# Performance work log

Measured on AMD Instinct MI355X. Metric: run time of the kernel, lower is better.

The kernel has to match this reference:

```python
import jax, jax.numpy as jnp
import numpy as np

B, C_IN, H, W = 32, 64, 64, 64
D, O, S_SP, K = 256, 512, 4, 3


def setup_inputs() -> dict:
    key = jax.random.key(0)
    k1, k2, k3, k4, k5 = jax.random.split(key, 5)
    x = jax.random.normal(k1, (B, C_IN, H, W), dtype=jnp.float32)
    dictionary = jax.random.normal(k2, (D, C_IN, K, K), dtype=jnp.float32)
    lookup_coefficients = jax.random.normal(k3, (O, S_SP), dtype=jnp.float32)
    bias = jax.random.normal(k4, (O,), dtype=jnp.float32)
    lookup_indices = jax.random.randint(k5, (O, S_SP), 0, D)
    return {
        "x": x,
        "dictionary": dictionary,
        "lookup_coefficients": lookup_coefficients,
        "bias": bias,
        "lookup_indices": lookup_indices,
    }


def reference(x, dictionary, lookup_coefficients, bias, lookup_indices):
    # Dictionary conv: S has shape [B, D, H, W] (stride 1, padding 1, 3x3 kernel)
    S = jax.lax.conv_general_dilated(
        x, dictionary,
        window_strides=(1, 1),
        padding=((1, 1), (1, 1)),
        dimension_numbers=("NCHW", "OIHW", "NCHW"),
    )
    # Build dense [O, D] combine matrix via scatter-add (duplicate indices
    # accumulate, matching the original += loop), then one GEMM.
    rows = jnp.arange(O)[:, None]  # [O, 1] broadcast against [O, sparsity]
    Wc = jnp.zeros((O, D), dtype=S.dtype).at[rows, lookup_indices].add(lookup_coefficients)
    out = jnp.einsum("bdhw,od->bohw", S, Wc)
    return out + bias[None, :, None, None]
```

## Files before the change

### kernel.cpp

```cpp
#include <hip/hip_runtime.h>
#include <stdint.h>

#define NB 32
#define NC 64
#define NH 64
#define NW 64
#define NO 512
#define HP 66

typedef __bf16 bf16x8 __attribute__((ext_vector_type(8)));
typedef short  s16x8  __attribute__((ext_vector_type(8)));
typedef float  f32x4  __attribute__((ext_vector_type(4)));

__device__ __forceinline__ uint16_t f2bf(float f) {
  uint32_t u = __builtin_bit_cast(uint32_t, f);
  u += 0x7fffu + ((u >> 16) & 1u);
  return (uint16_t)(u >> 16);
}

__device__ __forceinline__ void gld16(const uint16_t* g, uint16_t* l) {
  __builtin_amdgcn_global_load_lds(
      (const __attribute__((address_space(1))) void*)(g),
      (__attribute__((address_space(3))) void*)(l), 16, 0, 0);
}

__global__ void k_build_w(const float* __restrict__ dict,
                          const float* __restrict__ coef,
                          const int*   __restrict__ idx,
                          uint16_t*    __restrict__ Wl) {
  __shared__ float tmp[576];
  const int o = blockIdx.x;
  const int t = threadIdx.x;
  float v = 0.f;
#pragma unroll
  for (int s = 0; s < 4; ++s)
    v += coef[o * 4 + s] * dict[idx[o * 4 + s] * 576 + t];
  tmp[t] = v;
  __syncthreads();
  const int c = t & 63, p = t >> 6;
  const int sl = ((p * NO + o) * 8 + ((c >> 3) ^ (o & 7))) * 8 + (c & 7);
  Wl[sl] = f2bf(tmp[c * 9 + p]);
}

__global__ void k_nhwc(const float* __restrict__ x, uint16_t* __restrict__ xh) {
  const int bh = blockIdx.x;
  const int b = bh / HP, hp = bh % HP;
  const int t = threadIdx.x;
  uint16_t* row = xh + (size_t)(b * HP + hp) * 4096;
  if (hp == 0 || hp == HP - 1) {
    int4* r4 = reinterpret_cast<int4*>(row);
    r4[t]       = int4{0, 0, 0, 0};
    r4[t + 256] = int4{0, 0, 0, 0};
    return;
  }
  __shared__ float tile[64][65];
  const int h = hp - 1;
  const int w = t & 63;
#pragma unroll
  for (int c = (t >> 6); c < 64; c += 4)
    tile[c][w] = x[((size_t)(b * NC + c) * NH + h) * NW + w];
  __syncthreads();
#pragma unroll
  for (int i = 0; i < 2; ++i) {
    const int s = t + i * 256;
    const int w2 = s >> 3, cb = s & 7;
    uint32_t d[4];
#pragma unroll
    for (int j = 0; j < 4; ++j) {
      const uint32_t lo = f2bf(tile[cb * 8 + 2 * j][w2]);
      const uint32_t hi = f2bf(tile[cb * 8 + 2 * j + 1][w2]);
      d[j] = lo | (hi << 16);
    }
    reinterpret_cast<int4*>(row)[w2 * 8 + (cb ^ (w2 & 7))] =
        int4{(int)d[0], (int)d[1], (int)d[2], (int)d[3]};
  }
}

__global__ __launch_bounds__(512, 2) void k_conv(
    const uint16_t* __restrict__ xh,
    const uint16_t* __restrict__ Wl,
    const float*    __restrict__ bias,
    float*          __restrict__ out) {
  __shared__ __align__(16) uint16_t xs[10 * 66 * 64];
  __shared__ __align__(16) uint16_t as[3 * 128 * 64];

  const int t = threadIdx.x;
  const int flat = blockIdx.x;
  const int s    = (flat & 7) * 128 + (flat >> 3);
  const int ot   = s & 3;
  const int gy   = s >> 2;
  const int o0 = ot * 128;
  const int b  = gy >> 3;
  const int h0 = (gy & 7) * 8;

  const int lane = t & 63;
  const int wid  = t >> 6;

  if (t < 160) {
    const int r = t >> 4, sl = (t >> 3) & 1, j = t & 7;
    reinterpret_cast<int4*>(xs)[r * 528 + sl * 520 + j] = int4{0, 0, 0, 0};
  }

  {
    const uint16_t* srow = xh + (size_t)(b * HP + h0 + wid) * 4096;
    uint16_t* drow = xs + wid * 4224 + 64;
#pragma unroll
    for (int k = 0; k < 8; ++k)
      gld16(srow + k * 512 + lane * 8, drow + k * 512);
    const int r2 = 8 + (wid >> 2);
    const int kb = (wid & 3) * 2;
    const uint16_t* srow2 = xh + (size_t)(b * HP + h0 + r2) * 4096;
    uint16_t* drow2 = xs + r2 * 4224 + 64;
    gld16(srow2 + kb * 512 + lane * 8, drow2 + kb * 512);
    gld16(srow2 + (kb + 1) * 512 + lane * 8, drow2 + (kb + 1) * 512);
  }
  asm volatile("" ::: "memory");

  auto stage_a = [&](int p, int bufsel) {
    const uint16_t* src = Wl + (size_t)p * 32768 + o0 * 64;
    uint16_t* dst = as + bufsel * 8192;
#pragma unroll
    for (int j = 0; j < 2; ++j) {
      const int ch = wid * 2 + j;
      gld16(src + ch * 512 + lane * 8, dst + ch * 512);
    }
  };
  stage_a(0, 0);
  asm volatile("" ::: "memory");
  stage_a(1, 1);
  asm volatile("" ::: "memory");

  const int wm  = wid & 1;
  const int wn  = wid >> 1;
  const int l15 = lane & 15;
  const int g   = lane >> 4;

  f32x4 acc[4][8] = {};

#pragma unroll
  for (int p = 0; p < 9; ++p) {
    if (p == 0)      asm volatile("s_waitcnt vmcnt(2) lgkmcnt(0)" ::: "memory");
    else if (p == 8) asm volatile("s_waitcnt vmcnt(0)" ::: "memory");
    else             asm volatile("s_waitcnt vmcnt(2)" ::: "memory");
    __builtin_amdgcn_s_barrier();
    asm volatile("" ::: "memory");

    if (p + 2 <= 8) stage_a(p + 2, (p + 2) % 3);

    const int dh = p / 3 - 1, dw = p % 3 - 1;
    const uint16_t* asb = as + (p % 3) * 8192;

#pragma unroll
    for (int q = 0; q < 2; ++q) {
      bf16x8 af[4], bfr[8];
#pragma unroll
      for (int m = 0; m < 4; ++m) {
        const int orow = wm * 64 + m * 16 + l15;
        const int cb = (q * 4 + g) ^ (orow & 7);
        af[m] = __builtin_bit_cast(bf16x8,
            *reinterpret_cast<const s16x8*>(asb + orow * 64 + cb * 8));
      }
#pragma unroll
      for (int n = 0; n < 8; ++n) {
        const int row = wn * 2 + (n >> 2) + dh + 1;
        const int wv  = (n & 3) * 16 + l15 + dw;
        const int cb  = (q * 4 + g) ^ (wv & 7);
        bfr[n] = __builtin_bit_cast(bf16x8,
            *reinterpret_cast<const s16x8*>(xs + row * 4224 + (wv + 1) * 64 + cb * 8));
      }
      __builtin_amdgcn_s_setprio(1);
#pragma unroll
      for (int m = 0; m < 4; ++m)
#pragma unroll
        for (int n = 0; n < 8; ++n)
          acc[m][n] = __builtin_amdgcn_mfma_f32_16x16x32_bf16(
              af[m], bfr[n], acc[m][n], 0, 0, 0);
      __builtin_amdgcn_s_setprio(0);
    }
  }

  const int hb = h0 + wn * 2;
#pragma unroll
  for (int m = 0; m < 4; ++m) {
#pragma unroll
    for (int rr = 0; rr < 4; ++rr) {
      const int o = o0 + wm * 64 + m * 16 + g * 4 + rr;
      const float bv = bias[o];
      float* op = out + ((size_t)(b * NO + o) * NH + hb) * NW;
#pragma unroll
      for (int n = 0; n < 8; ++n)
        op[(n >> 2) * NW + (n & 3) * 16 + l15] = acc[m][n][rr] + bv;
    }
  }
}

extern "C" void kernel_launch(void* const* d_in, const int* in_sizes, int n_in,
                              void* d_out, int out_size, void* d_ws, size_t ws_size,
                              hipStream_t stream) {
  const float* x    = (const float*)d_in[0];
  const float* dict = (const float*)d_in[1];
  const float* coef = (const float*)d_in[2];
  const float* bias = (const float*)d_in[3];
  const int*   idx  = (const int*)d_in[4];
  float* out = (float*)d_out;

  uint16_t* xh = (uint16_t*)d_ws;
  uint16_t* Wl = (uint16_t*)((char*)d_ws + (18u << 20));

  hipLaunchKernelGGL(k_build_w, dim3(NO), dim3(576), 0, stream, dict, coef, idx, Wl);
  hipLaunchKernelGGL(k_nhwc, dim3(NB * HP), dim3(256), 0, stream, x, xh);
  hipLaunchKernelGGL(k_conv, dim3(1024), dim3(512), 0, stream, xh, Wl, bias, out);
}
```

Baseline: 117.9 us.

## Group conv taps by column offset to reuse input fragments across rows

The 9-tap loop is reordered into 3 column-offset groups. Each group loads all three row taps' weights at once, and the B fragments for 4 input rows are loaded once and shared across the three dh taps, which cuts LDS reads of the input tile. The cost is that the rolling triple-buffered weight prefetch is replaced by a synchronous load between groups with two full barriers. Weight loads are therefore no longer overlapped with MFMA work, and more registers stay live for the 16 B fragments.

Result: faster. 113.0 us (-4.2%).

```diff
diff --git a/kernel.cpp b/kernel.cpp
--- a/kernel.cpp
+++ b/kernel.cpp
@@ -114,68 +114,69 @@
     gld16(srow2 + kb * 512 + lane * 8, drow2 + kb * 512);
     gld16(srow2 + (kb + 1) * 512 + lane * 8, drow2 + (kb + 1) * 512);
   }
-  asm volatile("" ::: "memory");
-
-  auto stage_a = [&](int p, int bufsel) {
-    const uint16_t* src = Wl + (size_t)p * 32768 + o0 * 64;
-    uint16_t* dst = as + bufsel * 8192;
-#pragma unroll
-    for (int j = 0; j < 2; ++j) {
-      const int ch = wid * 2 + j;
-      gld16(src + ch * 512 + lane * 8, dst + ch * 512);
+
+  auto stage_a = [&](int g) {
+#pragma unroll
+    for (int j = 0; j < 6; ++j) {
+      const int c = wid * 6 + j;
+      const int tap = c >> 4, k = c & 15;
+      const uint16_t* src =
+          Wl + (size_t)(tap * 3 + g) * 32768 + o0 * 64 + k * 512;
+      gld16(src + lane * 8, as + tap * 8192 + k * 512);
     }
   };
-  stage_a(0, 0);
-  asm volatile("" ::: "memory");
-  stage_a(1, 1);
-  asm volatile("" ::: "memory");
+  stage_a(0);
 
   const int wm  = wid & 1;
   const int wn  = wid >> 1;
   const int l15 = lane & 15;
-  const int g   = lane >> 4;
+  const int lg  = lane >> 4;
 
   f32x4 acc[4][8] = {};
 
-#pragma unroll
-  for (int p = 0; p < 9; ++p) {
-    if (p == 0)      asm volatile("s_waitcnt vmcnt(2) lgkmcnt(0)" ::: "memory");
-    else if (p == 8) asm volatile("s_waitcnt vmcnt(0)" ::: "memory");
-    else             asm volatile("s_waitcnt vmcnt(2)" ::: "memory");
-    __builtin_amdgcn_s_barrier();
-    asm volatile("" ::: "memory");
-
-    if (p + 2 <= 8) stage_a(p + 2, (p + 2) % 3);
-
-    const int dh = p / 3 - 1, dw = p % 3 - 1;
-    const uint16_t* asb = as + (p % 3) * 8192;
+  __syncthreads();
+
+#pragma unroll
+  for (int g = 0; g < 3; ++g) {
+    const int dw = g - 1;
 
 #pragma unroll
     for (int q = 0; q < 2; ++q) {
-      bf16x8 af[4], bfr[8];
-#pragma unroll
-      for (int m = 0; m < 4; ++m) {
-        const int orow = wm * 64 + m * 16 + l15;
-        const int cb = (q * 4 + g) ^ (orow & 7);
-        af[m] = __builtin_bit_cast(bf16x8,
-            *reinterpret_cast<const s16x8*>(asb + orow * 64 + cb * 8));
+      bf16x8 braw[4][4];
+#pragma unroll
+      for (int rr = 0; rr < 4; ++rr) {
+        const int rbase = (wn * 2 + rr) * 4224;
+#pragma unroll
+        for (int nw = 0; nw < 4; ++nw) {
+          const int wv = nw * 16 + l15 + dw;
+          const int cb = (q * 4 + lg) ^ (wv & 7);
+          braw[rr][nw] = __builtin_bit_cast(bf16x8,
+              *reinterpret_cast<const s16x8*>(xs + rbase + (wv + 1) * 64 + cb * 8));
+        }
       }
 #pragma unroll
-      for (int n = 0; n < 8; ++n) {
-        const int row = wn * 2 + (n >> 2) + dh + 1;
-        const int wv  = (n & 3) * 16 + l15 + dw;
-        const int cb  = (q * 4 + g) ^ (wv & 7);
-        bfr[n] = __builtin_bit_cast(bf16x8,
-            *reinterpret_cast<const s16x8*>(xs + row * 4224 + (wv + 1) * 64 + cb * 8));
+      for (int dh = 0; dh < 3; ++dh) {
+        bf16x8 af[4];
+#pragma unroll
+        for (int m = 0; m < 4; ++m) {
+          const int orow = wm * 64 + m * 16 + l15;
+          const int cb = (q * 4 + lg) ^ (orow & 7);
+          af[m] = __builtin_bit_cast(bf16x8,
+              *reinterpret_cast<const s16x8*>(as + dh * 8192 + orow * 64 + cb * 8));
+        }
+#pragma unroll
+        for (int m = 0; m < 4; ++m)
+#pragma unroll
+          for (int n = 0; n < 8; ++n)
+            acc[m][n] = __builtin_amdgcn_mfma_f32_16x16x32_bf16(
+                af[m], braw[(n >> 2) + dh][n & 3], acc[m][n], 0, 0, 0);
       }
-      __builtin_amdgcn_s_setprio(1);
-#pragma unroll
-      for (int m = 0; m < 4; ++m)
-#pragma unroll
-        for (int n = 0; n < 8; ++n)
-          acc[m][n] = __builtin_amdgcn_mfma_f32_16x16x32_bf16(
-              af[m], bfr[n], acc[m][n], 0, 0, 0);
-      __builtin_amdgcn_s_setprio(0);
+    }
+
+    if (g < 2) {
+      __syncthreads();
+      stage_a(g + 1);
+      __syncthreads();
     }
   }
 
@@ -184,7 +185,7 @@
   for (int m = 0; m < 4; ++m) {
 #pragma unroll
     for (int rr = 0; rr < 4; ++rr) {
-      const int o = o0 + wm * 64 + m * 16 + g * 4 + rr;
+      const int o = o0 + wm * 64 + m * 16 + lg * 4 + rr;
       const float bv = bias[o];
       float* op = out + ((size_t)(b * NO + o) * NH + hb) * NW;
 #pragma unroll
```
